# Optimization experiments

Measured on AMD Instinct MI355X. Metric: run time of the kernel, lower is better.

Reference implementation:

```python
import jax, jax.numpy as jnp
import numpy as np

CLAMP_LO, CLAMP_HI = 1e-4, 1.0 - 1e-4
DELTA = 1.0

def setup_inputs() -> dict:
    key = jax.random.key(0)
    k1, = jax.random.split(key, 1)
    B, T, C = 32, 4096, 512
    x = jax.random.normal(k1, (B, T, C), dtype=jnp.float32)
    init_alpha = jnp.clip(jnp.float32(0.9), CLAMP_LO, CLAMP_HI)
    a0 = jnp.log(init_alpha) - jnp.log1p(-init_alpha)  # logit
    logit_alpha = jnp.full((C,), a0, dtype=jnp.float32)
    return {"x": x, "logit_alpha": logit_alpha}

def reference(x, logit_alpha):
    # x: [B, T, C]; logit_alpha: [C]
    a = jnp.clip(jax.nn.sigmoid(logit_alpha), CLAMP_LO, CLAMP_HI).astype(x.dtype)  # [C]
    d = jnp.asarray(DELTA, dtype=x.dtype)
    one_minus_a = 1.0 - a

    def step(y_prev, x_t):
        # y_prev, x_t: [B, C]
        r = x_t - y_prev
        g = jnp.where(jnp.abs(r) <= d, r, d * jnp.sign(r))  # Huber pseudo-gradient
        y_t = y_prev + one_minus_a * g
        return y_t, y_t

    y0 = x[:, 0, :]                      # [B, C]
    xs = jnp.swapaxes(x[:, 1:, :], 0, 1)  # [T-1, B, C]
    _, ys = jax.lax.scan(step, y0, xs)    # ys: [T-1, B, C]
    out = jnp.concatenate([y0[:, None, :], jnp.swapaxes(ys, 0, 1)], axis=1)  # [B, T, C]
    return out
```

## Files before the change

### kernel.cpp

```cpp
#include <hip/hip_runtime.h>
#include <math.h>


constexpr int B = 32;
constexpr int T = 4096;
constexpr int C = 512;
constexpr int SEG = 4;
constexpr int SEG_T = T / SEG;
constexpr int WARM = 256;

template <int U, bool STORE>
__device__ __forceinline__ float run_chunk(const float* __restrict__ xp,
                                           float* __restrict__ op,
                                           int t, float y, float oma) {
    float xv[U];
#pragma unroll
    for (int u = 0; u < U; ++u) {
        xv[u] = __builtin_nontemporal_load(xp + (size_t)(t + u) * C);
    }
#pragma unroll
    for (int u = 0; u < U; ++u) {
        float r = xv[u] - y;
        float g = fminf(1.0f, fmaxf(-1.0f, r));
        y = fmaf(oma, g, y);
        if (STORE) __builtin_nontemporal_store(y, op + (size_t)(t + u) * C);
    }
    return y;
}

__global__ __launch_bounds__(64, 1) void huber_ema_kernel(
    const float* __restrict__ x, const float* __restrict__ logit_alpha,
    float* __restrict__ out) {
    const int s = blockIdx.x >> 8;
    const int rem = blockIdx.x & 255;
    const int b = rem >> 3;
    const int c = ((rem & 7) << 6) + threadIdx.x;

    const float la = logit_alpha[c];
    float a = 1.0f / (1.0f + expf(-la));
    a = fminf(1.0f - 1e-4f, fmaxf(1e-4f, a));
    const float oma = 1.0f - a;

    const float* xp = x + (size_t)b * T * C + c;
    float* op = out + (size_t)b * T * C + c;

    const int t_begin = s * SEG_T;
    float y;
    int t;

    if (s == 0) {
        y = __builtin_nontemporal_load(xp);
        __builtin_nontemporal_store(y, op);
        t = 1;
#pragma unroll 1
        for (int i = 0; i < 31; ++i) {
            y = run_chunk<32, true>(xp, op, t, y, oma);
            t += 32;
        }
        y = run_chunk<31, true>(xp, op, t, y, oma);
    } else {
        const int t0 = t_begin - WARM;
        y = __builtin_nontemporal_load(xp + (size_t)t0 * C);
        t = t0 + 1;
#pragma unroll 1
        for (int i = 0; i < 7; ++i) {
            y = run_chunk<32, false>(xp, op, t, y, oma);
            t += 32;
        }
        y = run_chunk<31, false>(xp, op, t, y, oma);
        t += 31;
#pragma unroll 1
        for (int i = 0; i < 32; ++i) {
            y = run_chunk<32, true>(xp, op, t, y, oma);
            t += 32;
        }
    }
}

extern "C" void kernel_launch(void* const* d_in, const int* in_sizes, int n_in,
                              void* d_out, int out_size, void* d_ws, size_t ws_size,
                              hipStream_t stream) {
    const float* x = (const float*)d_in[0];
    const float* logit_alpha = (const float*)d_in[1];
    float* out = (float*)d_out;
    (void)in_sizes; (void)n_in; (void)out_size; (void)d_ws; (void)ws_size;

    dim3 grid(SEG * B * (C / 64));
    dim3 block(64);
    hipLaunchKernelGGL(huber_ema_kernel, grid, block, 0, stream, x, logit_alpha, out);
}
```

Before: 436.6 us.

## Double-buffer x loads across chunks and halve time segments with longer warmup

Adds a two-buffer software pipeline so the loads for the next chunk are issued while the current chunk's serial recurrence runs, hiding global memory latency. Time segmentation drops from 4 to 2, with warmup raised to 288 steps, which cuts redundant warmup reads but halves the number of blocks (1024 down to 512). Fewer waves in flight reduces parallelism for this latency-bound scan, and the doubled register buffers raise register use.

```diff
diff --git a/kernel.cpp b/kernel.cpp
--- a/kernel.cpp
+++ b/kernel.cpp
@@ -5,22 +5,42 @@
 constexpr int B = 32;
 constexpr int T = 4096;
 constexpr int C = 512;
-constexpr int SEG = 4;
+constexpr int SEG = 2;
 constexpr int SEG_T = T / SEG;
-constexpr int WARM = 256;
+constexpr int WARM = 288;
+constexpr int U = 32;
 
-template <int U, bool STORE>
-__device__ __forceinline__ float run_chunk(const float* __restrict__ xp,
-                                           float* __restrict__ op,
-                                           int t, float y, float oma) {
-    float xv[U];
+__device__ __forceinline__ void load_chunk(const float* __restrict__ xp, int t,
+                                           float (&v)[U]) {
+    t = (t > T - U) ? (T - U) : t;
+#pragma unroll
+    for (int u = 0; u < U; ++u)
+        v[u] = __builtin_nontemporal_load(xp + (size_t)(t + u) * C);
+}
+
+template <bool STORE>
+__device__ __forceinline__ float ema_chunk(float* __restrict__ op, int t,
+                                           const float (&v)[U], float y,
+                                           float oma) {
 #pragma unroll
     for (int u = 0; u < U; ++u) {
-        xv[u] = __builtin_nontemporal_load(xp + (size_t)(t + u) * C);
+        float r = v[u] - y;
+        float g = fminf(1.0f, fmaxf(-1.0f, r));
+        y = fmaf(oma, g, y);
+        if (STORE) __builtin_nontemporal_store(y, op + (size_t)(t + u) * C);
     }
+    return y;
+}
+
+template <bool STORE>
+__device__ __forceinline__ float ema_first_chunk(float* __restrict__ op, int t,
+                                                 const float (&v)[U],
+                                                 float oma) {
+    float y = v[0];
+    if (STORE) __builtin_nontemporal_store(y, op + (size_t)t * C);
 #pragma unroll
-    for (int u = 0; u < U; ++u) {
-        float r = xv[u] - y;
+    for (int u = 1; u < U; ++u) {
+        float r = v[u] - y;
         float g = fminf(1.0f, fmaxf(-1.0f, r));
         y = fmaf(oma, g, y);
         if (STORE) __builtin_nontemporal_store(y, op + (size_t)(t + u) * C);
@@ -44,35 +64,46 @@
     const float* xp = x + (size_t)b * T * C + c;
     float* op = out + (size_t)b * T * C + c;
 
-    const int t_begin = s * SEG_T;
+    float bufA[U], bufB[U];
     float y;
-    int t;
 
     if (s == 0) {
-        y = __builtin_nontemporal_load(xp);
-        __builtin_nontemporal_store(y, op);
-        t = 1;
+        load_chunk(xp, 0, bufA);
+        load_chunk(xp, U, bufB);
+        y = ema_first_chunk<true>(op, 0, bufA, oma);
+        load_chunk(xp, 2 * U, bufA);
+        int t = U;
 #pragma unroll 1
         for (int i = 0; i < 31; ++i) {
-            y = run_chunk<32, true>(xp, op, t, y, oma);
-            t += 32;
+            y = ema_chunk<true>(op, t, bufB, y, oma);
+            load_chunk(xp, t + 2 * U, bufB);
+            y = ema_chunk<true>(op, t + U, bufA, y, oma);
+            load_chunk(xp, t + 3 * U, bufA);
+            t += 2 * U;
         }
-        y = run_chunk<31, true>(xp, op, t, y, oma);
+        y = ema_chunk<true>(op, t, bufB, y, oma);
     } else {
-        const int t0 = t_begin - WARM;
-        y = __builtin_nontemporal_load(xp + (size_t)t0 * C);
-        t = t0 + 1;
+        const int t0 = SEG_T - WARM;
+        load_chunk(xp, t0, bufA);
+        load_chunk(xp, t0 + U, bufB);
+        y = ema_first_chunk<false>(op, t0, bufA, oma);
+        load_chunk(xp, t0 + 2 * U, bufA);
+        int t = t0 + U;
 #pragma unroll 1
-        for (int i = 0; i < 7; ++i) {
-            y = run_chunk<32, false>(xp, op, t, y, oma);
-            t += 32;
+        for (int i = 0; i < 4; ++i) {
+            y = ema_chunk<false>(op, t, bufB, y, oma);
+            load_chunk(xp, t + 2 * U, bufB);
+            y = ema_chunk<false>(op, t + U, bufA, y, oma);
+            load_chunk(xp, t + 3 * U, bufA);
+            t += 2 * U;
         }
-        y = run_chunk<31, false>(xp, op, t, y, oma);
-        t += 31;
 #pragma unroll 1
         for (int i = 0; i < 32; ++i) {
-            y = run_chunk<32, true>(xp, op, t, y, oma);
-            t += 32;
+            y = ema_chunk<true>(op, t, bufB, y, oma);
+            load_chunk(xp, t + 2 * U, bufB);
+            y = ema_chunk<true>(op, t + U, bufA, y, oma);
+            load_chunk(xp, t + 3 * U, bufA);
+            t += 2 * U;
         }
     }
 }
```

Result: no change. 429.9 us (-1.5%).
